# Kernel optimization log

Measured on AMD Instinct MI355X. Metric: run time of the kernel, lower is better.

The kernel has to match this reference:

```python
import jax, jax.numpy as jnp
import numpy as np
from jax import lax

# physiological constants from the source module
DT = 1.0
TAU_L = 10.0
G_B = 0.6
G_L = 1.0 / TAU_L
LAMBDA_MAX = 0.35
STEPS = int(50 / DT)

IN_SIZE, HID, OUT, BATCH = 1024, 2048, 512, 4096


def setup_inputs() -> dict:
    key = jax.random.key(0)
    k1, k2, k3, k4, k5, k6 = jax.random.split(key, 6)
    psp = jax.random.uniform(k1, (IN_SIZE, BATCH), dtype=jnp.float32)  # |mm(spikes,kernel)| is >=0
    label = jax.random.uniform(k2, (BATCH, OUT), dtype=jnp.float32)    # teaching current I
    # Linear params init: uniform(-0.1, 0.1) as in the torch module
    W_h = jax.random.uniform(k3, (HID, IN_SIZE), minval=-0.1, maxval=0.1, dtype=jnp.float32)
    b_h = jax.random.uniform(k4, (HID,), minval=-0.1, maxval=0.1, dtype=jnp.float32)
    W_o = jax.random.uniform(k5, (OUT, HID), minval=-0.1, maxval=0.1, dtype=jnp.float32)
    b_o = jax.random.uniform(k6, (OUT,), minval=-0.1, maxval=0.1, dtype=jnp.float32)
    return {"psp": psp, "label": label, "W_h": W_h, "b_h": b_h, "W_o": W_o, "b_o": b_o}


def reference(psp, label, W_h, b_h, W_o, b_o):
    a = DT / TAU_L
    gr = G_B / G_L  # = 6.0
    x = psp.T  # [B, in] -- Hidden_layer transposes basal_input
    # psp is constant over the time loop, so the hidden basal GEMM hoists out
    basal_V_h = x @ W_h.T + b_h  # [B, HID]
    soma_h0 = jnp.zeros_like(basal_V_h)
    soma_o0 = jnp.zeros((x.shape[0], W_o.shape[0]), dtype=x.dtype)

    def step(carry, _):
        soma_h, soma_o = carry
        # hidden two-compartment leaky integration
        soma_h = soma_h + a * (-soma_h + gr * (basal_V_h - soma_h))
        rate_h = LAMBDA_MAX * jax.nn.sigmoid(soma_h)  # [B, HID]
        basal_V_o = rate_h @ W_o.T + b_o              # [B, OUT]
        # output layer, training (test=False) branch: nudged by teaching current I=label
        soma_o = soma_o + a * (-soma_o + gr * (basal_V_o - soma_o) + label - soma_o)
        return (soma_h, soma_o), None

    (soma_h, soma_o), _ = lax.scan(step, (soma_h0, soma_o0), None, length=STEPS)
    return LAMBDA_MAX * jax.nn.sigmoid(soma_o)  # out_layer.spike_rate, [B, OUT]
```

## Files before the change

### kernel.cpp

```cpp
#include <hip/hip_runtime.h>
#include <hip/hip_bf16.h>


typedef __bf16 bf16_t;
typedef __bf16 bf16x8 __attribute__((ext_vector_type(8)));
typedef __bf16 bf16x4v __attribute__((ext_vector_type(4)));
typedef float f32x4 __attribute__((ext_vector_type(4)));

#define GLD_TO_LDS16(gp, lp)                                            \
  __builtin_amdgcn_global_load_lds(                                     \
      (__attribute__((address_space(1))) void*)(void*)(gp),             \
      (__attribute__((address_space(3))) void*)(lp), 16, 0, 0)

__global__ __launch_bounds__(256) void transpose_cvt(
    const float* __restrict__ in, bf16_t* __restrict__ out, int R, int C) {
  __shared__ float tile[64][65];
  const int tx = threadIdx.x & 63;
  const int ty = threadIdx.x >> 6;
  const int r0 = blockIdx.y * 64;
  const int c0 = blockIdx.x * 64;
#pragma unroll
  for (int i = 0; i < 16; ++i) {
    const int r = ty + i * 4;
    tile[r][tx] = in[(size_t)(r0 + r) * C + c0 + tx];
  }
  __syncthreads();
#pragma unroll
  for (int i = 0; i < 16; ++i) {
    const int r = ty + i * 4;
    out[(size_t)(c0 + r) * R + r0 + tx] = (bf16_t)tile[tx][r];
  }
}

__global__ __launch_bounds__(256) void cvt2_f32_bf16(
    const float4* __restrict__ w1, bf16x4v* __restrict__ o1, int n1,
    const float4* __restrict__ w2, bf16x4v* __restrict__ o2, int n2) {
  const int i = blockIdx.x * 256 + threadIdx.x;
  const float4 v = (i < n1) ? w1[i] : w2[i - n1];
  bf16x4v o;
  o.x = (bf16_t)v.x; o.y = (bf16_t)v.y; o.z = (bf16_t)v.z; o.w = (bf16_t)v.w;
  if (i < n1) o1[i] = o;
  else if (i - n1 < n2) o2[i - n1] = o;
}

__global__ __launch_bounds__(256, 2) void gemm1_nt(
    const bf16_t* __restrict__ A, const bf16_t* __restrict__ Bt,
    const float* __restrict__ bias, bf16_t* __restrict__ C,
    int M, int N, int K) {
  constexpr int BK = 64;
  __shared__ __align__(16) bf16_t sA[128 * BK];
  __shared__ __align__(16) bf16_t sB[128 * BK];

  const int tid = threadIdx.x;
  const int wave = tid >> 6;
  const int lane = tid & 63;
  const int bm = blockIdx.x * 128;
  const int bn = blockIdx.y * 128;
  const int wm = (wave & 1) * 64;
  const int wn = (wave >> 1) * 64;

  f32x4 acc[4][4] = {};

  const int srow8 = lane >> 3;
  const int gseg = (lane & 7) ^ srow8;
  const bf16_t* Ag = A + (size_t)(bm + wave * 32 + srow8) * K + gseg * 8;
  const bf16_t* Bg = Bt + (size_t)(bn + wave * 32 + srow8) * K + gseg * 8;
  const int dst = wave * 2048;

  const int fr = lane & 15;
  const int qh = lane >> 4;

  for (int k0 = 0; k0 < K; k0 += BK) {
#pragma unroll
    for (int c = 0; c < 4; ++c) {
      GLD_TO_LDS16(Ag + (size_t)(c * 8) * K + k0, sA + dst + c * 512);
      GLD_TO_LDS16(Bg + (size_t)(c * 8) * K + k0, sB + dst + c * 512);
    }
    __syncthreads();

#pragma unroll
    for (int ks = 0; ks < 2; ++ks) {
      const int q = ks * 4 + qh;
      bf16x8 av[4], bv[4];
#pragma unroll
      for (int i = 0; i < 4; ++i) {
        const int rr = wm + i * 16 + fr;
        av[i] = *(const bf16x8*)(sA + rr * BK + ((q ^ (rr & 7)) * 8));
      }
#pragma unroll
      for (int j = 0; j < 4; ++j) {
        const int rr = wn + j * 16 + fr;
        bv[j] = *(const bf16x8*)(sB + rr * BK + ((q ^ (rr & 7)) * 8));
      }
#pragma unroll
      for (int i = 0; i < 4; ++i)
#pragma unroll
        for (int j = 0; j < 4; ++j)
          acc[i][j] = __builtin_amdgcn_mfma_f32_16x16x32_bf16(
              av[i], bv[j], acc[i][j], 0, 0, 0);
    }
    __syncthreads();
  }

  const int cm0 = (lane >> 4) * 4;
#pragma unroll
  for (int j = 0; j < 4; ++j) {
    const int gn = bn + wn + j * 16 + fr;
    const float bj = bias[gn];
#pragma unroll
    for (int i = 0; i < 4; ++i) {
#pragma unroll
      for (int r = 0; r < 4; ++r) {
        const int gm = bm + wm + i * 16 + cm0 + r;
        const float z = 0.8571428571428571f * (acc[i][j][r] + bj);
        C[(size_t)gm * N + gn] = (bf16_t)(0.35f / (1.0f + __expf(-z)));
      }
    }
  }
}

__global__ __launch_bounds__(256, 4) void gemm2_nt(
    const bf16_t* __restrict__ A, const bf16_t* __restrict__ Bt,
    const float* __restrict__ bias, const float* __restrict__ lbl,
    float* __restrict__ out, int M, int N, int K) {
  constexpr int BK = 64;
  __shared__ __align__(16) bf16_t sA[64 * BK];
  __shared__ __align__(16) bf16_t sB[64 * BK];

  const int tid = threadIdx.x;
  const int wave = tid >> 6;
  const int lane = tid & 63;
  const int bm = blockIdx.x * 64;
  const int bn = blockIdx.y * 64;
  const int wm = (wave & 1) * 32;
  const int wn = (wave >> 1) * 32;

  f32x4 acc[2][2] = {};

  const int srow8 = lane >> 3;
  const int sseg0 = lane & 7;
  bf16_t* sAw = sA + wave * 1024;
  bf16_t* sBw = sB + wave * 1024;

  const int fr = lane & 15;
  const int qh = lane >> 4;

  for (int k0 = 0; k0 < K; k0 += BK) {
#pragma unroll
    for (int c = 0; c < 2; ++c) {
      const int row = (wave * 2 + c) * 8 + srow8;
      const int gseg = sseg0 ^ (row & 7);
      GLD_TO_LDS16(A + (size_t)(bm + row) * K + k0 + gseg * 8,
                   sAw + c * 512);
      GLD_TO_LDS16(Bt + (size_t)(bn + row) * K + k0 + gseg * 8,
                   sBw + c * 512);
    }
    __syncthreads();

#pragma unroll
    for (int ks = 0; ks < 2; ++ks) {
      const int q = ks * 4 + qh;
      bf16x8 av[2], bv[2];
#pragma unroll
      for (int i = 0; i < 2; ++i) {
        const int rr = wm + i * 16 + fr;
        av[i] = *(const bf16x8*)(sA + rr * BK + ((q ^ (rr & 7)) * 8));
      }
#pragma unroll
      for (int j = 0; j < 2; ++j) {
        const int rr = wn + j * 16 + fr;
        bv[j] = *(const bf16x8*)(sB + rr * BK + ((q ^ (rr & 7)) * 8));
      }
#pragma unroll
      for (int i = 0; i < 2; ++i)
#pragma unroll
        for (int j = 0; j < 2; ++j)
          acc[i][j] = __builtin_amdgcn_mfma_f32_16x16x32_bf16(
              av[i], bv[j], acc[i][j], 0, 0, 0);
    }
    __syncthreads();
  }

  const int cm0 = (lane >> 4) * 4;
#pragma unroll
  for (int j = 0; j < 2; ++j) {
    const int gn = bn + wn + j * 16 + fr;
    const float bj = bias[gn];
#pragma unroll
    for (int i = 0; i < 2; ++i) {
#pragma unroll
      for (int r = 0; r < 4; ++r) {
        const int gm = bm + wm + i * 16 + cm0 + r;
        const float z =
            0.75f * (acc[i][j][r] + bj) + 0.125f * lbl[(size_t)gm * N + gn];
        out[(size_t)gm * N + gn] = 0.35f / (1.0f + __expf(-z));
      }
    }
  }
}

extern "C" void kernel_launch(void* const* d_in, const int* in_sizes, int n_in,
                              void* d_out, int out_size, void* d_ws, size_t ws_size,
                              hipStream_t stream) {
  constexpr int IN = 1024, HID = 2048, OUT = 512, B = 4096;
  const float* psp = (const float*)d_in[0];
  const float* lbl = (const float*)d_in[1];
  const float* W_h = (const float*)d_in[2];
  const float* b_h = (const float*)d_in[3];
  const float* W_o = (const float*)d_in[4];
  const float* b_o = (const float*)d_in[5];
  float* out = (float*)d_out;

  bf16_t* Whb = (bf16_t*)d_ws;
  bf16_t* Wob = Whb + (size_t)HID * IN;
  bf16_t* pspT = Wob + (size_t)OUT * HID;
  bf16_t* Rm = pspT + (size_t)B * IN;

  transpose_cvt<<<dim3(B / 64, IN / 64), 256, 0, stream>>>(psp, pspT, IN, B);
  {
    const int n1 = HID * IN / 4, n2 = OUT * HID / 4;
    cvt2_f32_bf16<<<(n1 + n2 + 255) / 256, 256, 0, stream>>>(
        (const float4*)W_h, (bf16x4v*)Whb, n1,
        (const float4*)W_o, (bf16x4v*)Wob, n2);
  }
  gemm1_nt<<<dim3(B / 128, HID / 128), 256, 0, stream>>>(
      pspT, Whb, b_h, Rm, B, HID, IN);
  gemm2_nt<<<dim3(B / 64, OUT / 64), 256, 0, stream>>>(
      Rm, Wob, b_o, lbl, out, B, OUT, HID);
}
```

Baseline: 136.3 us.

## Fuse transpose, convert and both GEMMs into one persistent kernel with grid barriers

Replaces the four kernel launches with a single persistent kernel of 512 blocks. The transpose, weight conversion, first GEMM and second GEMM run as phases separated by atomic-counter grid barriers, with a memset resetting the counter first. The aim is to remove launch gaps and tail effects between the stages. In exchange, all blocks must be co-resident (2 per CU with 256 CUs), the second GEMM uses only 512 tiles, and every barrier waits on the slowest block.

Result: slower. 273.6 us (+100.8%).

```diff
diff --git a/kernel.cpp b/kernel.cpp
--- a/kernel.cpp
+++ b/kernel.cpp
@@ -12,188 +12,204 @@
       (__attribute__((address_space(1))) void*)(void*)(gp),             \
       (__attribute__((address_space(3))) void*)(lp), 16, 0, 0)
 
-__global__ __launch_bounds__(256) void transpose_cvt(
-    const float* __restrict__ in, bf16_t* __restrict__ out, int R, int C) {
-  __shared__ float tile[64][65];
-  const int tx = threadIdx.x & 63;
-  const int ty = threadIdx.x >> 6;
-  const int r0 = blockIdx.y * 64;
-  const int c0 = blockIdx.x * 64;
-#pragma unroll
-  for (int i = 0; i < 16; ++i) {
-    const int r = ty + i * 4;
-    tile[r][tx] = in[(size_t)(r0 + r) * C + c0 + tx];
-  }
+__device__ __forceinline__ void grid_barrier(unsigned* ctr, unsigned target) {
   __syncthreads();
-#pragma unroll
-  for (int i = 0; i < 16; ++i) {
-    const int r = ty + i * 4;
-    out[(size_t)(c0 + r) * R + r0 + tx] = (bf16_t)tile[tx][r];
-  }
+  if (threadIdx.x == 0) {
+    __threadfence();
+    __hip_atomic_fetch_add(ctr, 1u, __ATOMIC_ACQ_REL, __HIP_MEMORY_SCOPE_AGENT);
+    while (__hip_atomic_load(ctr, __ATOMIC_ACQUIRE, __HIP_MEMORY_SCOPE_AGENT) <
+           target) {
+      __builtin_amdgcn_s_sleep(2);
+    }
+    __threadfence();
+  }
+  __syncthreads();
 }
 
-__global__ __launch_bounds__(256) void cvt2_f32_bf16(
-    const float4* __restrict__ w1, bf16x4v* __restrict__ o1, int n1,
-    const float4* __restrict__ w2, bf16x4v* __restrict__ o2, int n2) {
-  const int i = blockIdx.x * 256 + threadIdx.x;
-  const float4 v = (i < n1) ? w1[i] : w2[i - n1];
-  bf16x4v o;
-  o.x = (bf16_t)v.x; o.y = (bf16_t)v.y; o.z = (bf16_t)v.z; o.w = (bf16_t)v.w;
-  if (i < n1) o1[i] = o;
-  else if (i - n1 < n2) o2[i - n1] = o;
-}
-
-__global__ __launch_bounds__(256, 2) void gemm1_nt(
-    const bf16_t* __restrict__ A, const bf16_t* __restrict__ Bt,
-    const float* __restrict__ bias, bf16_t* __restrict__ C,
-    int M, int N, int K) {
-  constexpr int BK = 64;
-  __shared__ __align__(16) bf16_t sA[128 * BK];
-  __shared__ __align__(16) bf16_t sB[128 * BK];
-
+__global__ __launch_bounds__(256, 2) void fused_all(
+    const float* __restrict__ psp,
+    const float* __restrict__ Wh,
+    const float* __restrict__ Wo,
+    const float* __restrict__ bh,
+    const float* __restrict__ bo,
+    const float* __restrict__ lbl,
+    bf16_t* __restrict__ pspT,
+    bf16_t* __restrict__ Whb,
+    bf16_t* __restrict__ Wob,
+    bf16_t* __restrict__ Rm,
+    float* __restrict__ out,
+    unsigned* __restrict__ ctr) {
+  __shared__ __align__(16) char smem[32768];
   const int tid = threadIdx.x;
+  const int b = blockIdx.x;
   const int wave = tid >> 6;
   const int lane = tid & 63;
-  const int bm = blockIdx.x * 128;
-  const int bn = blockIdx.y * 128;
-  const int wm = (wave & 1) * 64;
-  const int wn = (wave >> 1) * 64;
-
-  f32x4 acc[4][4] = {};
-
-  const int srow8 = lane >> 3;
-  const int gseg = (lane & 7) ^ srow8;
-  const bf16_t* Ag = A + (size_t)(bm + wave * 32 + srow8) * K + gseg * 8;
-  const bf16_t* Bg = Bt + (size_t)(bn + wave * 32 + srow8) * K + gseg * 8;
-  const int dst = wave * 2048;
+
+  {
+    float(*tile)[65] = (float(*)[65])smem;
+    const int tx = tid & 63;
+    const int ty = tid >> 6;
+#pragma unroll
+    for (int tt = 0; tt < 2; ++tt) {
+      const int t = b * 2 + tt;
+      const int c0 = (t & 63) * 64;
+      const int r0 = (t >> 6) * 64;
+      if (tt) __syncthreads();
+#pragma unroll
+      for (int i = 0; i < 16; ++i) {
+        const int r = ty + i * 4;
+        tile[r][tx] = psp[(size_t)(r0 + r) * 4096 + c0 + tx];
+      }
+      __syncthreads();
+#pragma unroll
+      for (int i = 0; i < 16; ++i) {
+        const int r = ty + i * 4;
+        pspT[(size_t)(c0 + r) * 1024 + r0 + tx] = (bf16_t)tile[tx][r];
+      }
+    }
+    const int base = b * 1536 + tid;
+#pragma unroll
+    for (int i = 0; i < 6; ++i) {
+      const int idx = base + i * 256;
+      const float4 v = (idx < 524288) ? ((const float4*)Wh)[idx]
+                                      : ((const float4*)Wo)[idx - 524288];
+      bf16x4v o;
+      o.x = (bf16_t)v.x; o.y = (bf16_t)v.y;
+      o.z = (bf16_t)v.z; o.w = (bf16_t)v.w;
+      if (idx < 524288) ((bf16x4v*)Whb)[idx] = o;
+      else ((bf16x4v*)Wob)[idx - 524288] = o;
+    }
+  }
+  grid_barrier(ctr, 512);
 
   const int fr = lane & 15;
   const int qh = lane >> 4;
-
-  for (int k0 = 0; k0 < K; k0 += BK) {
-#pragma unroll
-    for (int c = 0; c < 4; ++c) {
-      GLD_TO_LDS16(Ag + (size_t)(c * 8) * K + k0, sA + dst + c * 512);
-      GLD_TO_LDS16(Bg + (size_t)(c * 8) * K + k0, sB + dst + c * 512);
-    }
-    __syncthreads();
-
-#pragma unroll
-    for (int ks = 0; ks < 2; ++ks) {
-      const int q = ks * 4 + qh;
-      bf16x8 av[4], bv[4];
+  const int srow8 = lane >> 3;
+  const int gsegw = (lane & 7) ^ srow8;
+  const int cm0 = (lane >> 4) * 4;
+
+  {
+    bf16_t* sA = (bf16_t*)smem;
+    bf16_t* sB = sA + 128 * 64;
+    const int bm = (b & 31) * 128;
+    const int bn = (b >> 5) * 128;
+    const int wm = (wave & 1) * 64;
+    const int wn = (wave >> 1) * 64;
+
+    f32x4 acc[4][4] = {};
+    const bf16_t* Ag = pspT + (size_t)(bm + wave * 32 + srow8) * 1024 + gsegw * 8;
+    const bf16_t* Bg = Whb + (size_t)(bn + wave * 32 + srow8) * 1024 + gsegw * 8;
+    const int dst = wave * 2048;
+
+    for (int k0 = 0; k0 < 1024; k0 += 64) {
+#pragma unroll
+      for (int c = 0; c < 4; ++c) {
+        GLD_TO_LDS16(Ag + (size_t)(c * 8) * 1024 + k0, sA + dst + c * 512);
+        GLD_TO_LDS16(Bg + (size_t)(c * 8) * 1024 + k0, sB + dst + c * 512);
+      }
+      __syncthreads();
+#pragma unroll
+      for (int ks = 0; ks < 2; ++ks) {
+        const int q = ks * 4 + qh;
+        bf16x8 av[4], bv[4];
+#pragma unroll
+        for (int i = 0; i < 4; ++i) {
+          const int rr = wm + i * 16 + fr;
+          av[i] = *(const bf16x8*)(sA + rr * 64 + ((q ^ (rr & 7)) * 8));
+        }
+#pragma unroll
+        for (int j = 0; j < 4; ++j) {
+          const int rr = wn + j * 16 + fr;
+          bv[j] = *(const bf16x8*)(sB + rr * 64 + ((q ^ (rr & 7)) * 8));
+        }
+#pragma unroll
+        for (int i = 0; i < 4; ++i)
+#pragma unroll
+          for (int j = 0; j < 4; ++j)
+            acc[i][j] = __builtin_amdgcn_mfma_f32_16x16x32_bf16(
+                av[i], bv[j], acc[i][j], 0, 0, 0);
+      }
+      __syncthreads();
+    }
+
+#pragma unroll
+    for (int j = 0; j < 4; ++j) {
+      const int gn = bn + wn + j * 16 + fr;
+      const float bj = bh[gn];
 #pragma unroll
       for (int i = 0; i < 4; ++i) {
-        const int rr = wm + i * 16 + fr;
-        av[i] = *(const bf16x8*)(sA + rr * BK + ((q ^ (rr & 7)) * 8));
-      }
-#pragma unroll
-      for (int j = 0; j < 4; ++j) {
-        const int rr = wn + j * 16 + fr;
-        bv[j] = *(const bf16x8*)(sB + rr * BK + ((q ^ (rr & 7)) * 8));
-      }
-#pragma unroll
-      for (int i = 0; i < 4; ++i)
-#pragma unroll
-        for (int j = 0; j < 4; ++j)
-          acc[i][j] = __builtin_amdgcn_mfma_f32_16x16x32_bf16(
-              av[i], bv[j], acc[i][j], 0, 0, 0);
-    }
-    __syncthreads();
-  }
-
-  const int cm0 = (lane >> 4) * 4;
-#pragma unroll
-  for (int j = 0; j < 4; ++j) {
-    const int gn = bn + wn + j * 16 + fr;
-    const float bj = bias[gn];
-#pragma unroll
-    for (int i = 0; i < 4; ++i) {
-#pragma unroll
-      for (int r = 0; r < 4; ++r) {
-        const int gm = bm + wm + i * 16 + cm0 + r;
-        const float z = 0.8571428571428571f * (acc[i][j][r] + bj);
-        C[(size_t)gm * N + gn] = (bf16_t)(0.35f / (1.0f + __expf(-z)));
-      }
-    }
-  }
-}
-
-__global__ __launch_bounds__(256, 4) void gemm2_nt(
-    const bf16_t* __restrict__ A, const bf16_t* __restrict__ Bt,
-    const float* __restrict__ bias, const float* __restrict__ lbl,
-    float* __restrict__ out, int M, int N, int K) {
-  constexpr int BK = 64;
-  __shared__ __align__(16) bf16_t sA[64 * BK];
-  __shared__ __align__(16) bf16_t sB[64 * BK];
-
-  const int tid = threadIdx.x;
-  const int wave = tid >> 6;
-  const int lane = tid & 63;
-  const int bm = blockIdx.x * 64;
-  const int bn = blockIdx.y * 64;
-  const int wm = (wave & 1) * 32;
-  const int wn = (wave >> 1) * 32;
-
-  f32x4 acc[2][2] = {};
-
-  const int srow8 = lane >> 3;
-  const int sseg0 = lane & 7;
-  bf16_t* sAw = sA + wave * 1024;
-  bf16_t* sBw = sB + wave * 1024;
-
-  const int fr = lane & 15;
-  const int qh = lane >> 4;
-
-  for (int k0 = 0; k0 < K; k0 += BK) {
-#pragma unroll
-    for (int c = 0; c < 2; ++c) {
-      const int row = (wave * 2 + c) * 8 + srow8;
-      const int gseg = sseg0 ^ (row & 7);
-      GLD_TO_LDS16(A + (size_t)(bm + row) * K + k0 + gseg * 8,
-                   sAw + c * 512);
-      GLD_TO_LDS16(Bt + (size_t)(bn + row) * K + k0 + gseg * 8,
-                   sBw + c * 512);
-    }
-    __syncthreads();
-
-#pragma unroll
-    for (int ks = 0; ks < 2; ++ks) {
-      const int q = ks * 4 + qh;
-      bf16x8 av[2], bv[2];
+#pragma unroll
+        for (int r = 0; r < 4; ++r) {
+          const int gm = bm + wm + i * 16 + cm0 + r;
+          const float z = 0.8571428571428571f * (acc[i][j][r] + bj);
+          Rm[(size_t)gm * 2048 + gn] = (bf16_t)(0.35f / (1.0f + __expf(-z)));
+        }
+      }
+    }
+  }
+  grid_barrier(ctr, 1024);
+
+  {
+    bf16_t* sA = (bf16_t*)smem;
+    bf16_t* sB = sA + 64 * 64;
+    const int bm = (b & 63) * 64;
+    const int bn = (b >> 6) * 64;
+    const int wm = (wave & 1) * 32;
+    const int wn = (wave >> 1) * 32;
+
+    f32x4 acc[2][2] = {};
+    const int sseg0 = lane & 7;
+    bf16_t* sAw = sA + wave * 1024;
+    bf16_t* sBw = sB + wave * 1024;
+
+    for (int k0 = 0; k0 < 2048; k0 += 64) {
+#pragma unroll
+      for (int c = 0; c < 2; ++c) {
+        const int row = (wave * 2 + c) * 8 + srow8;
+        const int gseg = sseg0 ^ (row & 7);
+        GLD_TO_LDS16(Rm + (size_t)(bm + row) * 2048 + k0 + gseg * 8,
+                     sAw + c * 512);
+        GLD_TO_LDS16(Wob + (size_t)(bn + row) * 2048 + k0 + gseg * 8,
+                     sBw + c * 512);
+      }
+      __syncthreads();
+#pragma unroll
+      for (int ks = 0; ks < 2; ++ks) {
+        const int q = ks * 4 + qh;
+        bf16x8 av[2], bv[2];
+#pragma unroll
+        for (int i = 0; i < 2; ++i) {
+          const int rr = wm + i * 16 + fr;
+          av[i] = *(const bf16x8*)(sA + rr * 64 + ((q ^ (rr & 7)) * 8));
+        }
+#pragma unroll
+        for (int j = 0; j < 2; ++j) {
+          const int rr = wn + j * 16 + fr;
+          bv[j] = *(const bf16x8*)(sB + rr * 64 + ((q ^ (rr & 7)) * 8));
+        }
+#pragma unroll
+        for (int i = 0; i < 2; ++i)
+#pragma unroll
+          for (int j = 0; j < 2; ++j)
+            acc[i][j] = __builtin_amdgcn_mfma_f32_16x16x32_bf16(
+                av[i], bv[j], acc[i][j], 0, 0, 0);
+      }
+      __syncthreads();
+    }
+
+#pragma unroll
+    for (int j = 0; j < 2; ++j) {
+      const int gn = bn + wn + j * 16 + fr;
+      const float bj = bo[gn];
 #pragma unroll
       for (int i = 0; i < 2; ++i) {
-        const int rr = wm + i * 16 + fr;
-        av[i] = *(const bf16x8*)(sA + rr * BK + ((q ^ (rr & 7)) * 8));
-      }
-#pragma unroll
-      for (int j = 0; j < 2; ++j) {
-        const int rr = wn + j * 16 + fr;
-        bv[j] = *(const bf16x8*)(sB + rr * BK + ((q ^ (rr & 7)) * 8));
-      }
-#pragma unroll
-      for (int i = 0; i < 2; ++i)
-#pragma unroll
-        for (int j = 0; j < 2; ++j)
-          acc[i][j] = __builtin_amdgcn_mfma_f32_16x16x32_bf16(
-              av[i], bv[j], acc[i][j], 0, 0, 0);
-    }
-    __syncthreads();
-  }
-
-  const int cm0 = (lane >> 4) * 4;
-#pragma unroll
-  for (int j = 0; j < 2; ++j) {
-    const int gn = bn + wn + j * 16 + fr;
-    const float bj = bias[gn];
-#pragma unroll
-    for (int i = 0; i < 2; ++i) {
-#pragma unroll
-      for (int r = 0; r < 4; ++r) {
-        const int gm = bm + wm + i * 16 + cm0 + r;
-        const float z =
-            0.75f * (acc[i][j][r] + bj) + 0.125f * lbl[(size_t)gm * N + gn];
-        out[(size_t)gm * N + gn] = 0.35f / (1.0f + __expf(-z));
+#pragma unroll
+        for (int r = 0; r < 4; ++r) {
+          const int gm = bm + wm + i * 16 + cm0 + r;
+          const float z =
+              0.75f * (acc[i][j][r] + bj) + 0.125f * lbl[(size_t)gm * 512 + gn];
+          out[(size_t)gm * 512 + gn] = 0.35f / (1.0f + __expf(-z));
+        }
       }
     }
   }
@@ -215,16 +231,9 @@
   bf16_t* Wob = Whb + (size_t)HID * IN;
   bf16_t* pspT = Wob + (size_t)OUT * HID;
   bf16_t* Rm = pspT + (size_t)B * IN;
-
-  transpose_cvt<<<dim3(B / 64, IN / 64), 256, 0, stream>>>(psp, pspT, IN, B);
-  {
-    const int n1 = HID * IN / 4, n2 = OUT * HID / 4;
-    cvt2_f32_bf16<<<(n1 + n2 + 255) / 256, 256, 0, stream>>>(
-        (const float4*)W_h, (bf16x4v*)Whb, n1,
-        (const float4*)W_o, (bf16x4v*)Wob, n2);
-  }
-  gemm1_nt<<<dim3(B / 128, HID / 128), 256, 0, stream>>>(
-      pspT, Whb, b_h, Rm, B, HID, IN);
-  gemm2_nt<<<dim3(B / 64, OUT / 64), 256, 0, stream>>>(
-      Rm, Wob, b_o, lbl, out, B, OUT, HID);
+  unsigned* ctr = (unsigned*)(Rm + (size_t)B * HID);
+
+  hipMemsetAsync(ctr, 0, 128, stream);
+  fused_all<<<512, 256, 0, stream>>>(psp, W_h, W_o, b_h, b_o, lbl,
+                                     pspT, Whb, Wob, Rm, out, ctr);
 }
```
